# Kernel optimization log

Measured on AMD Instinct MI355X. Metric: run time of the kernel, lower is better.

The kernel has to match this reference:

```python
import math
import jax, jax.numpy as jnp
import numpy as np

LMAX = 2


def _cg_complex(j1, m1, j2, m2, j3, m3):
    # Standard (Racah) Clebsch-Gordan coefficient <j1 m1 j2 m2 | j3 m3> for integer l.
    if m1 + m2 != m3 or j3 < abs(j1 - j2) or j3 > j1 + j2:
        return 0.0
    f = math.factorial
    pre = math.sqrt((2 * j3 + 1) * f(j3 + j1 - j2) * f(j3 - j1 + j2) * f(j1 + j2 - j3) / f(j1 + j2 + j3 + 1))
    pre *= math.sqrt(f(j3 + m3) * f(j3 - m3) * f(j1 - m1) * f(j1 + m1) * f(j2 - m2) * f(j2 + m2))
    kmin = max(0, j2 - j3 - m1, j1 + m2 - j3)
    kmax = min(j1 + j2 - j3, j1 - m1, j2 + m2)
    s = 0.0
    for k in range(kmin, kmax + 1):
        s += (-1.0) ** k / (f(k) * f(j1 + j2 - j3 - k) * f(j1 - m1 - k) * f(j2 + m2 - k) * f(j3 - j2 + m1 + k) * f(j3 - j1 - m2 + k))
    return pre * s


def _u_matrix(l):
    # Unitary map from complex SH (Condon-Shortley) to real SH, rows = real mu, cols = complex m.
    U = np.zeros((2 * l + 1, 2 * l + 1), dtype=np.complex128)
    U[l, l] = 1.0
    isq2 = 1.0 / math.sqrt(2.0)
    for m in range(1, l + 1):
        U[l + m, l - m] = isq2
        U[l + m, l + m] = ((-1.0) ** m) * isq2
        U[l - m, l - m] = 1j * isq2
        U[l - m, l + m] = -1j * ((-1.0) ** m) * isq2
    return U


def _real_clebsch_gordan(lmax):
    # Dense real-SH CG tensor over combined s=(l,m) indices, shape [S,S,S], S=(lmax+1)^2.
    S = (lmax + 1) ** 2
    cg = np.zeros((S, S, S))
    for l1 in range(lmax + 1):
        for l2 in range(lmax + 1):
            for l3 in range(abs(l1 - l2), min(lmax, l1 + l2) + 1):
                blk = np.zeros((2 * l1 + 1, 2 * l2 + 1, 2 * l3 + 1))
                for i1, m1 in enumerate(range(-l1, l1 + 1)):
                    for i2, m2 in enumerate(range(-l2, l2 + 1)):
                        for i3, m3 in enumerate(range(-l3, l3 + 1)):
                            blk[i1, i2, i3] = _cg_complex(l1, m1, l2, m2, l3, m3)
                U1, U2, U3 = _u_matrix(l1), _u_matrix(l2), _u_matrix(l3)
                r = np.einsum('am,bn,co,mno->abc', U1, U2, U3.conj(), blk.astype(np.complex128))
                r = r.real if (l1 + l2 + l3) % 2 == 0 else r.imag  # parity-dependent real part
                cg[l1 * l1:(l1 + 1) ** 2, l2 * l2:(l2 + 1) ** 2, l3 * l3:(l3 + 1) ** 2] = r
    return cg


def _sparse_cg(lmax):
    cg = _real_clebsch_gordan(lmax)
    i1, i2, i3 = np.nonzero(np.abs(cg) > 1e-10)
    vals = cg[i1, i2, i3].astype(np.float32)
    widx = np.floor(np.sqrt(i3.astype(np.float64))).astype(np.int32)  # l of output combined index
    return vals, i1.astype(np.int32), i2.astype(np.int32), i3.astype(np.int32), widx


def _spherical_harmonics_l2(d):
    # Real SH up to l=2, 'component' normalization (|x|=1 assumed). Order: (l,m) = (0,0),(1,-1),(1,0),(1,1),(2,-2..2).
    x, y, z = d[..., 0], d[..., 1], d[..., 2]
    s3, s5, s15 = math.sqrt(3.0), math.sqrt(5.0), math.sqrt(15.0)
    return jnp.stack([
        jnp.ones_like(x),
        s3 * y, s3 * z, s3 * x,
        s15 * x * y, s15 * y * z, 0.5 * s5 * (3.0 * z * z - 1.0), s15 * x * z, 0.5 * s15 * (x * x - y * y),
    ], axis=-1)


def setup_inputs():
    N_ATOMS, N_EDGES, N_BASIS, N_RADIAL = 1200, 12000, 128, 20
    S = (LMAX + 1) ** 2
    key = jax.random.key(0)
    ks = jax.random.split(key, 8)
    vals, i1, i2, i3, widx = _sparse_cg(LMAX)
    return {
        'x': jax.random.normal(ks[0], (N_ATOMS, S, N_BASIS), jnp.float32),
        'radial_ij': jax.random.uniform(ks[1], (N_EDGES, N_RADIAL), jnp.float32),
        'dir_ij': jax.random.normal(ks[2], (N_EDGES, 3), jnp.float32),
        'cutoff_ij': jax.random.uniform(ks[3], (N_EDGES, 1), jnp.float32),
        'W_filter': jax.random.normal(ks[6], (N_RADIAL, N_BASIS * (LMAX + 1)), jnp.float32) / math.sqrt(N_RADIAL),
        'b_filter': jnp.zeros((N_BASIS * (LMAX + 1),), jnp.float32),
        'cg_vals': jnp.asarray(vals),
        'idx_i': jax.random.randint(ks[4], (N_EDGES,), 0, N_ATOMS),
        'idx_j': jax.random.randint(ks[5], (N_EDGES,), 0, N_ATOMS),
        'cg_idx_in1': jnp.asarray(i1),
        'cg_idx_in2': jnp.asarray(i2),
        'cg_idx_out': jnp.asarray(i3),
        'w_idx': jnp.asarray(widx),
    }


def reference(x, radial_ij, dir_ij, cutoff_ij, W_filter, b_filter, cg_vals,
              idx_i, idx_j, cg_idx_in1, cg_idx_in2, cg_idx_out, w_idx):
    n_atoms, S, F = x.shape
    E = dir_ij.shape[0]
    d = dir_ij / jnp.linalg.norm(dir_ij, axis=-1, keepdims=True)
    Y = _spherical_harmonics_l2(d)                        # [E, S]
    Wij = (radial_ij @ W_filter + b_filter) * cutoff_ij   # [E, (lmax+1)*F]
    Wij = Wij.reshape(E, LMAX + 1, F)                     # per-l radial filter
    xj = x[idx_j]                                         # [E, S, F] neighbor features
    # Sparse CG tensor-product contraction over combined (l,m) indices.
    v = (Y[:, cg_idx_in2, None] * cg_vals[None, :, None]
         * Wij[:, w_idx, :] * xj[:, cg_idx_in1, :])       # [E, n_cg, F]
    yij = jnp.zeros((E, S, F), v.dtype).at[:, cg_idx_out, :].add(v)
    return jax.ops.segment_sum(yij, idx_i, num_segments=n_atoms)
```

## Files before the change

### kernel.cpp

```cpp
#include <hip/hip_runtime.h>
#include <math.h>


#define S9     9
#define MROW   12
#define NF     128
#define NRAD   20
#define CEDGE  8

__device__ inline float2 f2fma(float a, float2 b, float2 c) {
    return make_float2(fmaf(a, b.x, c.x), fmaf(a, b.y, c.y));
}

__global__ void hist_kernel(const int* __restrict__ idx_i, int E, int* __restrict__ counts) {
    int e = blockIdx.x * blockDim.x + threadIdx.x;
    if (e < E) atomicAdd(&counts[idx_i[e]], 1);
}

__global__ __launch_bounds__(256) void scan_kernel(const int* __restrict__ counts, int A,
                                                   int* __restrict__ offsets, int* __restrict__ cursor,
                                                   int* __restrict__ chunk_off) {
    __shared__ int part[256];
    const int t = threadIdx.x;
    const int base = t * 8;
    int c[8];
    int s = 0;
    #pragma unroll
    for (int p = 0; p < 8; ++p) {
        int idx = base + p;
        c[p] = (idx < A) ? counts[idx] : 0;
        s += c[p];
    }
    part[t] = s;
    __syncthreads();
    #pragma unroll
    for (int off = 1; off < 256; off <<= 1) {
        int v = (t >= off) ? part[t - off] : 0;
        __syncthreads();
        part[t] += v;
        __syncthreads();
    }
    int run = part[t] - s;
    #pragma unroll
    for (int p = 0; p < 8; ++p) {
        int idx = base + p;
        if (idx < A) { offsets[idx] = run; cursor[idx] = run; run += c[p]; }
    }
    if (t == 255) offsets[A] = run;
    __syncthreads();

    int k[8];
    int s2 = 0;
    #pragma unroll
    for (int p = 0; p < 8; ++p) {
        int idx = base + p;
        k[p] = (idx < A) ? ((c[p] + CEDGE - 1) / CEDGE) : 0;
        s2 += k[p];
    }
    part[t] = s2;
    __syncthreads();
    #pragma unroll
    for (int off = 1; off < 256; off <<= 1) {
        int v = (t >= off) ? part[t - off] : 0;
        __syncthreads();
        part[t] += v;
        __syncthreads();
    }
    int run2 = part[t] - s2;
    #pragma unroll
    for (int p = 0; p < 8; ++p) {
        int idx = base + p;
        if (idx < A) { chunk_off[idx] = run2; run2 += k[p]; }
    }
    if (t == 255) chunk_off[A] = run2;
}

__global__ void scatter_kernel(const int* __restrict__ idx_i, int E,
                               int* __restrict__ cursor, int* __restrict__ esorted) {
    int e = blockIdx.x * blockDim.x + threadIdx.x;
    if (e < E) {
        int p = atomicAdd(&cursor[idx_i[e]], 1);
        esorted[p] = e;
    }
}

__global__ __launch_bounds__(64) void so3_chunk_kernel(
    const float* __restrict__ x,
    const float* __restrict__ radial,
    const float* __restrict__ dir,
    const float* __restrict__ cutoff,
    const float* __restrict__ Wf,
    const float* __restrict__ bf,
    const float* __restrict__ cg_vals,
    const int* __restrict__ idx_j,
    const int* __restrict__ cg_i1,
    const int* __restrict__ cg_i2,
    const int* __restrict__ cg_i3,
    int ncg, int A,
    const int* __restrict__ offsets,
    const int* __restrict__ chunk_off,
    const int* __restrict__ esorted,
    float* __restrict__ slots,
    float* __restrict__ out,
    int use_slots)
{
    const int ch = blockIdx.x;
    const int nchunks = chunk_off[A];
    if (ch >= nchunks) return;

    int lo = 0, hi = A;
    while (hi - lo > 1) {
        int mid = (lo + hi) >> 1;
        if (chunk_off[mid] <= ch) lo = mid; else hi = mid;
    }
    const int a = lo;
    const int q = ch - chunk_off[a];
    const int estart = offsets[a] + q * CEDGE;
    const int n = min(CEDGE, offsets[a + 1] - estart);

    const int t = threadIdx.x;

    __shared__ __align__(16) float M[CEDGE][MROW * S9];
    __shared__ float Ysh[CEDGE][S9];
    __shared__ int   els[CEDGE];

    {
        float4* Mz = (float4*)&M[0][0];
        const int tot4 = CEDGE * MROW * S9 / 4;
        for (int qq = t; qq < tot4; qq += 64) Mz[qq] = make_float4(0.f, 0.f, 0.f, 0.f);
    }
    if (t < n) {
        const int e = esorted[estart + t];
        els[t] = e;
        float dx = dir[3 * e], dy = dir[3 * e + 1], dz = dir[3 * e + 2];
        const float inv = rsqrtf(dx * dx + dy * dy + dz * dz);
        dx *= inv; dy *= inv; dz *= inv;
        const float s3c  = 1.7320508075688772f;
        const float s5c  = 2.2360679774997896f;
        const float s15c = 3.8729833462074170f;
        Ysh[t][0] = 1.0f;
        Ysh[t][1] = s3c * dy;
        Ysh[t][2] = s3c * dz;
        Ysh[t][3] = s3c * dx;
        Ysh[t][4] = s15c * dx * dy;
        Ysh[t][5] = s15c * dy * dz;
        Ysh[t][6] = 0.5f * s5c * (3.0f * dz * dz - 1.0f);
        Ysh[t][7] = s15c * dx * dz;
        Ysh[t][8] = 0.5f * s15c * (dx * dx - dy * dy);
    }
    __syncthreads();

    {
        const int c = t >> 3;
        const int r = t & 7;
        if (c < n) {
            for (int kk = r; kk < ncg; kk += 8) {
                atomicAdd(&M[c][cg_i3[kk] * MROW + cg_i1[kk]], cg_vals[kk] * Ysh[c][cg_i2[kk]]);
            }
        }
    }
    __syncthreads();

    float2 acc[S9];
    #pragma unroll
    for (int s = 0; s < S9; ++s) acc[s] = make_float2(0.f, 0.f);

    const float2 b0 = ((const float2*)(bf + 0 * NF))[t];
    const float2 b1 = ((const float2*)(bf + 1 * NF))[t];
    const float2 b2 = ((const float2*)(bf + 2 * NF))[t];

    for (int c = 0; c < n; ++c) {
        int e = __builtin_amdgcn_readfirstlane(els[c]);
        const int j = __builtin_amdgcn_readfirstlane(idx_j[e]);
        const float cut = cutoff[e];

        float rad[NRAD];
        #pragma unroll
        for (int r = 0; r < NRAD; ++r) rad[r] = radial[e * NRAD + r];

        float2 wl0 = b0, wl1 = b1, wl2 = b2;
        #pragma unroll
        for (int r = 0; r < NRAD; ++r) {
            const float2* wrow = (const float2*)(Wf + r * (3 * NF));
            wl0 = f2fma(rad[r], wrow[t],            wl0);
            wl1 = f2fma(rad[r], wrow[t + 64],       wl1);
            wl2 = f2fma(rad[r], wrow[t + 128],      wl2);
        }
        wl0.x *= cut; wl0.y *= cut; wl1.x *= cut; wl1.y *= cut; wl2.x *= cut; wl2.y *= cut;

        const float2* xp = (const float2*)(x + (size_t)j * (S9 * NF)) + t;
        float2 xj[S9];
        #pragma unroll
        for (int s = 0; s < S9; ++s) xj[s] = xp[s * 64];

        #pragma unroll
        for (int s3 = 0; s3 < S9; ++s3) {
            const float4* mr = (const float4*)&M[c][s3 * MROW];
            const float4 m0 = mr[0];
            const float4 m1 = mr[1];
            const float  m8 = M[c][s3 * MROW + 8];
            float2 tsum = make_float2(0.f, 0.f);
            tsum = f2fma(m0.x, xj[0], tsum);
            tsum = f2fma(m0.y, xj[1], tsum);
            tsum = f2fma(m0.z, xj[2], tsum);
            tsum = f2fma(m0.w, xj[3], tsum);
            tsum = f2fma(m1.x, xj[4], tsum);
            tsum = f2fma(m1.y, xj[5], tsum);
            tsum = f2fma(m1.z, xj[6], tsum);
            tsum = f2fma(m1.w, xj[7], tsum);
            tsum = f2fma(m8,   xj[8], tsum);
            const float2 w = (s3 == 0) ? wl0 : ((s3 < 4) ? wl1 : wl2);
            acc[s3].x = fmaf(w.x, tsum.x, acc[s3].x);
            acc[s3].y = fmaf(w.y, tsum.y, acc[s3].y);
        }
    }

    if (use_slots) {
        float2* sp = (float2*)(slots + (size_t)ch * (S9 * NF)) + t;
        #pragma unroll
        for (int s = 0; s < S9; ++s) sp[s * 64] = acc[s];
    } else {
        float* op = out + (size_t)a * (S9 * NF) + 2 * t;
        #pragma unroll
        for (int s = 0; s < S9; ++s) {
            atomicAdd(&op[s * NF],     acc[s].x);
            atomicAdd(&op[s * NF + 1], acc[s].y);
        }
    }
}

__global__ __launch_bounds__(64) void so3_reduce_kernel(
    const float* __restrict__ slots, const int* __restrict__ chunk_off,
    float* __restrict__ out)
{
    const int a = blockIdx.x;
    const int t = threadIdx.x;
    const int c0 = chunk_off[a];
    const int c1 = chunk_off[a + 1];

    float2 acc[S9];
    #pragma unroll
    for (int s = 0; s < S9; ++s) acc[s] = make_float2(0.f, 0.f);

    for (int ch = c0; ch < c1; ++ch) {
        const float2* sp = (const float2*)(slots + (size_t)ch * (S9 * NF)) + t;
        #pragma unroll
        for (int s = 0; s < S9; ++s) {
            float2 v = sp[s * 64];
            acc[s].x += v.x; acc[s].y += v.y;
        }
    }
    float2* op = (float2*)(out + (size_t)a * (S9 * NF)) + t;
    #pragma unroll
    for (int s = 0; s < S9; ++s) op[s * 64] = acc[s];
}

extern "C" void kernel_launch(void* const* d_in, const int* in_sizes, int n_in,
                              void* d_out, int out_size, void* d_ws, size_t ws_size,
                              hipStream_t stream) {
    const float* x       = (const float*)d_in[0];
    const float* radial  = (const float*)d_in[1];
    const float* dir     = (const float*)d_in[2];
    const float* cutoff  = (const float*)d_in[3];
    const float* Wf      = (const float*)d_in[4];
    const float* bf      = (const float*)d_in[5];
    const float* cg_vals = (const float*)d_in[6];
    const int*   idx_i   = (const int*)d_in[7];
    const int*   idx_j   = (const int*)d_in[8];
    const int*   cg_i1   = (const int*)d_in[9];
    const int*   cg_i2   = (const int*)d_in[10];
    const int*   cg_i3   = (const int*)d_in[11];

    const int E   = in_sizes[7];
    const int ncg = in_sizes[6];
    const int A   = in_sizes[0] / (S9 * NF);

    int* counts    = (int*)d_ws;
    int* offsets   = counts + A;
    int* cursor    = offsets + (A + 1);
    int* chunk_off = cursor + A;
    int* esorted   = chunk_off + (A + 1);
    size_t int_bytes = (size_t)(4 * A + 2 + E) * sizeof(int);
    size_t slots_off = (int_bytes + 255) & ~(size_t)255;

    const int max_chunks = E / CEDGE + A;
    size_t slots_bytes = (size_t)max_chunks * (S9 * NF) * sizeof(float);
    const int use_slots = (ws_size >= slots_off + slots_bytes) ? 1 : 0;
    float* slots = (float*)((char*)d_ws + slots_off);
    float* out   = (float*)d_out;

    hipMemsetAsync(counts, 0, (size_t)A * sizeof(int), stream);

    const int TB = 256;
    hist_kernel<<<(E + TB - 1) / TB, TB, 0, stream>>>(idx_i, E, counts);
    scan_kernel<<<1, 256, 0, stream>>>(counts, A, offsets, cursor, chunk_off);
    scatter_kernel<<<(E + TB - 1) / TB, TB, 0, stream>>>(idx_i, E, cursor, esorted);

    if (!use_slots) {
        hipMemsetAsync(out, 0, (size_t)out_size * sizeof(float), stream);
    }

    so3_chunk_kernel<<<max_chunks, 64, 0, stream>>>(
        x, radial, dir, cutoff, Wf, bf, cg_vals, idx_j,
        cg_i1, cg_i2, cg_i3, ncg, A, offsets, chunk_off, esorted,
        slots, out, use_slots);

    if (use_slots) {
        so3_reduce_kernel<<<A, 64, 0, stream>>>(slots, chunk_off, out);
    }
}
```

Before: 125.5 us.

## Fuse CSR build into one block, batch radial filter, fold reduction into chunk kernel

Replaces the memset, histogram, scan and scatter launches with a single 1024-thread block that builds the CSR in shared memory, zeroes the outputs of atoms with no edges and resets the per-atom done counters. The chunk kernel now computes the radial filter for all 8 edges at once from shared radial data, so each Wf row is loaded once per chunk rather than once per edge. The separate reduce kernel is removed: atoms with one chunk write their output directly, and otherwise the last chunk to finish, found through an atomic done counter, sums the slots. This trades launch overhead and a kernel for a serial single-block preprocessing step and more register pressure from holding w[8][3], and the shared arrays limit A to 2048.

After: 193.1 us. 1.54x slower.

```diff
diff --git a/kernel.cpp b/kernel.cpp
--- a/kernel.cpp
+++ b/kernel.cpp
@@ -7,79 +7,82 @@
 #define NF     128
 #define NRAD   20
 #define CEDGE  8
+#define MAXA   2048
 
 __device__ inline float2 f2fma(float a, float2 b, float2 c) {
     return make_float2(fmaf(a, b.x, c.x), fmaf(a, b.y, c.y));
 }
 
-__global__ void hist_kernel(const int* __restrict__ idx_i, int E, int* __restrict__ counts) {
-    int e = blockIdx.x * blockDim.x + threadIdx.x;
-    if (e < E) atomicAdd(&counts[idx_i[e]], 1);
-}
-
-__global__ __launch_bounds__(256) void scan_kernel(const int* __restrict__ counts, int A,
-                                                   int* __restrict__ offsets, int* __restrict__ cursor,
-                                                   int* __restrict__ chunk_off) {
-    __shared__ int part[256];
+__global__ __launch_bounds__(1024) void csr_kernel(
+    const int* __restrict__ idx_i, int E, int A,
+    int* __restrict__ offsets,
+    int* __restrict__ chunk_off,
+    int* __restrict__ esorted,
+    int* __restrict__ done,
+    float* __restrict__ out)
+{
+    __shared__ int lcnt[MAXA];
+    __shared__ int lcur[MAXA];
+    __shared__ int part[1024];
     const int t = threadIdx.x;
-    const int base = t * 8;
-    int c[8];
-    int s = 0;
-    #pragma unroll
-    for (int p = 0; p < 8; ++p) {
-        int idx = base + p;
-        c[p] = (idx < A) ? counts[idx] : 0;
-        s += c[p];
-    }
-    part[t] = s;
-    __syncthreads();
-    #pragma unroll
-    for (int off = 1; off < 256; off <<= 1) {
+
+    for (int i = t; i < A; i += 1024) lcnt[i] = 0;
+    __syncthreads();
+    for (int e = t; e < E; e += 1024) atomicAdd(&lcnt[idx_i[e]], 1);
+    __syncthreads();
+
+    const int i0 = 2 * t, i1 = 2 * t + 1;
+    const int ca = (i0 < A) ? lcnt[i0] : 0;
+    const int cb = (i1 < A) ? lcnt[i1] : 0;
+
+    part[t] = ca + cb;
+    __syncthreads();
+    for (int off = 1; off < 1024; off <<= 1) {
         int v = (t >= off) ? part[t - off] : 0;
         __syncthreads();
         part[t] += v;
         __syncthreads();
     }
-    int run = part[t] - s;
-    #pragma unroll
-    for (int p = 0; p < 8; ++p) {
-        int idx = base + p;
-        if (idx < A) { offsets[idx] = run; cursor[idx] = run; run += c[p]; }
-    }
-    if (t == 255) offsets[A] = run;
-    __syncthreads();
-
-    int k[8];
-    int s2 = 0;
-    #pragma unroll
-    for (int p = 0; p < 8; ++p) {
-        int idx = base + p;
-        k[p] = (idx < A) ? ((c[p] + CEDGE - 1) / CEDGE) : 0;
-        s2 += k[p];
-    }
-    part[t] = s2;
-    __syncthreads();
-    #pragma unroll
-    for (int off = 1; off < 256; off <<= 1) {
+    int run = part[t] - (ca + cb);
+    if (i0 < A) { offsets[i0] = run; lcur[i0] = run; run += ca; }
+    if (i1 < A) { offsets[i1] = run; lcur[i1] = run; run += cb; }
+    if (t == 1023) offsets[A] = run;
+    __syncthreads();
+
+    const int ka = (i0 < A) ? ((ca + CEDGE - 1) / CEDGE) : 0;
+    const int kb = (i1 < A) ? ((cb + CEDGE - 1) / CEDGE) : 0;
+    part[t] = ka + kb;
+    __syncthreads();
+    for (int off = 1; off < 1024; off <<= 1) {
         int v = (t >= off) ? part[t - off] : 0;
         __syncthreads();
         part[t] += v;
         __syncthreads();
     }
-    int run2 = part[t] - s2;
-    #pragma unroll
-    for (int p = 0; p < 8; ++p) {
-        int idx = base + p;
-        if (idx < A) { chunk_off[idx] = run2; run2 += k[p]; }
-    }
-    if (t == 255) chunk_off[A] = run2;
-}
-
-__global__ void scatter_kernel(const int* __restrict__ idx_i, int E,
-                               int* __restrict__ cursor, int* __restrict__ esorted) {
-    int e = blockIdx.x * blockDim.x + threadIdx.x;
-    if (e < E) {
-        int p = atomicAdd(&cursor[idx_i[e]], 1);
+    int run2 = part[t] - (ka + kb);
+    if (i0 < A) { chunk_off[i0] = run2; run2 += ka; }
+    if (i1 < A) { chunk_off[i1] = run2; run2 += kb; }
+    if (t == 1023) chunk_off[A] = run2;
+
+    const float4 z4 = make_float4(0.f, 0.f, 0.f, 0.f);
+    if (i0 < A) {
+        done[i0] = 0;
+        if (ca == 0) {
+            float4* o = (float4*)(out + (size_t)i0 * (S9 * NF));
+            for (int s = 0; s < S9 * NF / 4; ++s) o[s] = z4;
+        }
+    }
+    if (i1 < A) {
+        done[i1] = 0;
+        if (cb == 0) {
+            float4* o = (float4*)(out + (size_t)i1 * (S9 * NF));
+            for (int s = 0; s < S9 * NF / 4; ++s) o[s] = z4;
+        }
+    }
+    __syncthreads();
+
+    for (int e = t; e < E; e += 1024) {
+        int p = atomicAdd(&lcur[idx_i[e]], 1);
         esorted[p] = e;
     }
 }
@@ -101,6 +104,7 @@
     const int* __restrict__ chunk_off,
     const int* __restrict__ esorted,
     float* __restrict__ slots,
+    int* __restrict__ done,
     float* __restrict__ out,
     int use_slots)
 {
@@ -114,7 +118,9 @@
         if (chunk_off[mid] <= ch) lo = mid; else hi = mid;
     }
     const int a = lo;
-    const int q = ch - chunk_off[a];
+    const int c0ch = chunk_off[a];
+    const int c1ch = chunk_off[a + 1];
+    const int q = ch - c0ch;
     const int estart = offsets[a] + q * CEDGE;
     const int n = min(CEDGE, offsets[a + 1] - estart);
 
@@ -122,6 +128,8 @@
 
     __shared__ __align__(16) float M[CEDGE][MROW * S9];
     __shared__ float Ysh[CEDGE][S9];
+    __shared__ float radsh[CEDGE][NRAD];
+    __shared__ float cutsh[CEDGE];
     __shared__ int   els[CEDGE];
 
     {
@@ -148,7 +156,41 @@
         Ysh[t][7] = s15c * dx * dz;
         Ysh[t][8] = 0.5f * s15c * (dx * dx - dy * dy);
     }
-    __syncthreads();
+    if (t < CEDGE) cutsh[t] = (t < n) ? cutoff[esorted[estart + t]] : 0.f;
+    for (int qq = t; qq < CEDGE * NRAD; qq += 64) {
+        const int c = qq / NRAD;
+        const int r = qq - c * NRAD;
+        radsh[c][r] = (c < n) ? radial[(size_t)esorted[estart + c] * NRAD + r] : 0.f;
+    }
+    __syncthreads();
+
+    const float2 b0 = ((const float2*)(bf + 0 * NF))[t];
+    const float2 b1 = ((const float2*)(bf + 1 * NF))[t];
+    const float2 b2 = ((const float2*)(bf + 2 * NF))[t];
+    float2 w[CEDGE][3];
+    #pragma unroll
+    for (int c = 0; c < CEDGE; ++c) { w[c][0] = b0; w[c][1] = b1; w[c][2] = b2; }
+    #pragma unroll 4
+    for (int r = 0; r < NRAD; ++r) {
+        const float2* wrow = (const float2*)(Wf + r * (3 * NF));
+        const float2 w0 = wrow[t];
+        const float2 w1 = wrow[t + 64];
+        const float2 w2 = wrow[t + 128];
+        #pragma unroll
+        for (int c = 0; c < CEDGE; ++c) {
+            const float rv = radsh[c][r];
+            w[c][0] = f2fma(rv, w0, w[c][0]);
+            w[c][1] = f2fma(rv, w1, w[c][1]);
+            w[c][2] = f2fma(rv, w2, w[c][2]);
+        }
+    }
+    #pragma unroll
+    for (int c = 0; c < CEDGE; ++c) {
+        const float cut = cutsh[c];
+        w[c][0].x *= cut; w[c][0].y *= cut;
+        w[c][1].x *= cut; w[c][1].y *= cut;
+        w[c][2].x *= cut; w[c][2].y *= cut;
+    }
 
     {
         const int c = t >> 3;
@@ -165,28 +207,11 @@
     #pragma unroll
     for (int s = 0; s < S9; ++s) acc[s] = make_float2(0.f, 0.f);
 
-    const float2 b0 = ((const float2*)(bf + 0 * NF))[t];
-    const float2 b1 = ((const float2*)(bf + 1 * NF))[t];
-    const float2 b2 = ((const float2*)(bf + 2 * NF))[t];
-
-    for (int c = 0; c < n; ++c) {
-        int e = __builtin_amdgcn_readfirstlane(els[c]);
+    #pragma unroll
+    for (int c = 0; c < CEDGE; ++c) {
+        if (c >= n) break;
+        const int e = __builtin_amdgcn_readfirstlane(els[c]);
         const int j = __builtin_amdgcn_readfirstlane(idx_j[e]);
-        const float cut = cutoff[e];
-
-        float rad[NRAD];
-        #pragma unroll
-        for (int r = 0; r < NRAD; ++r) rad[r] = radial[e * NRAD + r];
-
-        float2 wl0 = b0, wl1 = b1, wl2 = b2;
-        #pragma unroll
-        for (int r = 0; r < NRAD; ++r) {
-            const float2* wrow = (const float2*)(Wf + r * (3 * NF));
-            wl0 = f2fma(rad[r], wrow[t],            wl0);
-            wl1 = f2fma(rad[r], wrow[t + 64],       wl1);
-            wl2 = f2fma(rad[r], wrow[t + 128],      wl2);
-        }
-        wl0.x *= cut; wl0.y *= cut; wl1.x *= cut; wl1.y *= cut; wl2.x *= cut; wl2.y *= cut;
 
         const float2* xp = (const float2*)(x + (size_t)j * (S9 * NF)) + t;
         float2 xj[S9];
@@ -209,50 +234,52 @@
             tsum = f2fma(m1.z, xj[6], tsum);
             tsum = f2fma(m1.w, xj[7], tsum);
             tsum = f2fma(m8,   xj[8], tsum);
-            const float2 w = (s3 == 0) ? wl0 : ((s3 < 4) ? wl1 : wl2);
-            acc[s3].x = fmaf(w.x, tsum.x, acc[s3].x);
-            acc[s3].y = fmaf(w.y, tsum.y, acc[s3].y);
-        }
-    }
-
-    if (use_slots) {
-        float2* sp = (float2*)(slots + (size_t)ch * (S9 * NF)) + t;
-        #pragma unroll
-        for (int s = 0; s < S9; ++s) sp[s * 64] = acc[s];
-    } else {
+            const float2 wl = (s3 == 0) ? w[c][0] : ((s3 < 4) ? w[c][1] : w[c][2]);
+            acc[s3].x = fmaf(wl.x, tsum.x, acc[s3].x);
+            acc[s3].y = fmaf(wl.y, tsum.y, acc[s3].y);
+        }
+    }
+
+    if (!use_slots) {
         float* op = out + (size_t)a * (S9 * NF) + 2 * t;
         #pragma unroll
         for (int s = 0; s < S9; ++s) {
             atomicAdd(&op[s * NF],     acc[s].x);
             atomicAdd(&op[s * NF + 1], acc[s].y);
         }
-    }
-}
-
-__global__ __launch_bounds__(64) void so3_reduce_kernel(
-    const float* __restrict__ slots, const int* __restrict__ chunk_off,
-    float* __restrict__ out)
-{
-    const int a = blockIdx.x;
-    const int t = threadIdx.x;
-    const int c0 = chunk_off[a];
-    const int c1 = chunk_off[a + 1];
-
-    float2 acc[S9];
-    #pragma unroll
-    for (int s = 0; s < S9; ++s) acc[s] = make_float2(0.f, 0.f);
-
-    for (int ch = c0; ch < c1; ++ch) {
-        const float2* sp = (const float2*)(slots + (size_t)ch * (S9 * NF)) + t;
-        #pragma unroll
-        for (int s = 0; s < S9; ++s) {
-            float2 v = sp[s * 64];
-            acc[s].x += v.x; acc[s].y += v.y;
-        }
-    }
-    float2* op = (float2*)(out + (size_t)a * (S9 * NF)) + t;
-    #pragma unroll
-    for (int s = 0; s < S9; ++s) op[s * 64] = acc[s];
+        return;
+    }
+
+    const int nch = c1ch - c0ch;
+    if (nch == 1) {
+        float2* op = (float2*)(out + (size_t)a * (S9 * NF)) + t;
+        #pragma unroll
+        for (int s = 0; s < S9; ++s) op[s * 64] = acc[s];
+        return;
+    }
+
+    float2* sp = (float2*)(slots + (size_t)ch * (S9 * NF)) + t;
+    #pragma unroll
+    for (int s = 0; s < S9; ++s) sp[s * 64] = acc[s];
+    __threadfence();
+    int old = 0;
+    if (t == 0) old = atomicAdd(&done[a], 1);
+    old = __shfl(old, 0);
+    if (old == nch - 1) {
+        __threadfence();
+        for (int ch2 = c0ch; ch2 < c1ch; ++ch2) {
+            if (ch2 == ch) continue;
+            const float2* rp = (const float2*)(slots + (size_t)ch2 * (S9 * NF)) + t;
+            #pragma unroll
+            for (int s = 0; s < S9; ++s) {
+                float2 v = rp[s * 64];
+                acc[s].x += v.x; acc[s].y += v.y;
+            }
+        }
+        float2* op = (float2*)(out + (size_t)a * (S9 * NF)) + t;
+        #pragma unroll
+        for (int s = 0; s < S9; ++s) op[s * 64] = acc[s];
+    }
 }
 
 extern "C" void kernel_launch(void* const* d_in, const int* in_sizes, int n_in,
@@ -275,12 +302,11 @@
     const int ncg = in_sizes[6];
     const int A   = in_sizes[0] / (S9 * NF);
 
-    int* counts    = (int*)d_ws;
-    int* offsets   = counts + A;
-    int* cursor    = offsets + (A + 1);
-    int* chunk_off = cursor + A;
-    int* esorted   = chunk_off + (A + 1);
-    size_t int_bytes = (size_t)(4 * A + 2 + E) * sizeof(int);
+    int* offsets   = (int*)d_ws;
+    int* chunk_off = offsets + (A + 1);
+    int* done      = chunk_off + (A + 1);
+    int* esorted   = done + A;
+    size_t int_bytes = (size_t)(3 * A + 2 + E) * sizeof(int);
     size_t slots_off = (int_bytes + 255) & ~(size_t)255;
 
     const int max_chunks = E / CEDGE + A;
@@ -289,23 +315,14 @@
     float* slots = (float*)((char*)d_ws + slots_off);
     float* out   = (float*)d_out;
 
-    hipMemsetAsync(counts, 0, (size_t)A * sizeof(int), stream);
-
-    const int TB = 256;
-    hist_kernel<<<(E + TB - 1) / TB, TB, 0, stream>>>(idx_i, E, counts);
-    scan_kernel<<<1, 256, 0, stream>>>(counts, A, offsets, cursor, chunk_off);
-    scatter_kernel<<<(E + TB - 1) / TB, TB, 0, stream>>>(idx_i, E, cursor, esorted);
-
     if (!use_slots) {
         hipMemsetAsync(out, 0, (size_t)out_size * sizeof(float), stream);
     }
+
+    csr_kernel<<<1, 1024, 0, stream>>>(idx_i, E, A, offsets, chunk_off, esorted, done, out);
 
     so3_chunk_kernel<<<max_chunks, 64, 0, stream>>>(
         x, radial, dir, cutoff, Wf, bf, cg_vals, idx_j,
         cg_i1, cg_i2, cg_i3, ncg, A, offsets, chunk_off, esorted,
-        slots, out, use_slots);
-
-    if (use_slots) {
-        so3_reduce_kernel<<<A, 64, 0, stream>>>(slots, chunk_off, out);
-    }
+        slots, done, out, use_slots);
 }
```
